# Kernel optimization log

Measured on AMD Instinct MI355X. Metric: run time of the kernel, lower is better.

Reference implementation:

```python
import jax, jax.numpy as jnp
import numpy as np

B, S, H, NH = 2, 2048, 2048, 16
HD = H // NH
CLIP_QKV = 8.0
SOFTMAX_SCALE = 1.0 / np.sqrt(HD)
NEG_INF = jnp.finfo(jnp.float32).min


def setup_inputs() -> dict:
    key = jax.random.key(0)
    k1, k2, k3, k4 = jax.random.split(key, 4)
    hidden_states = jax.random.normal(k1, (B, S, H), dtype=jnp.float32)
    position_bias = jax.random.normal(k2, (NH, S, S), dtype=jnp.float32) * 0.1
    # causal mask: True = masked out (upper triangle)
    causal = ~jnp.tril(jnp.ones((S, S), dtype=bool))
    attention_mask = jnp.broadcast_to(causal[None, None], (B, 1, S, S))
    Wqkv = jax.random.normal(k3, (3 * H, H), dtype=jnp.float32) * (1.0 / np.sqrt(H))
    Wout = jax.random.normal(k4, (H, H), dtype=jnp.float32) * (1.0 / np.sqrt(H))
    return {"hidden_states": hidden_states, "position_bias": position_bias,
            "attention_mask": attention_mask, "Wqkv": Wqkv, "Wout": Wout}


def reference(hidden_states, position_bias, attention_mask, Wqkv, Wout):
    # QKV projection (no bias) + clamp
    mixed = hidden_states @ Wqkv.T                        # [B,S,3H]
    mixed = jnp.clip(mixed, -CLIP_QKV, CLIP_QKV)
    q, k, v = jnp.split(mixed, 3, axis=2)
    # [B,S,H] -> [B,NH,S,HD]
    def split_heads(x):
        return x.reshape(B, S, NH, HD).transpose(0, 2, 1, 3)
    q, k, v = split_heads(q), split_heads(k), split_heads(v)
    scores = jnp.einsum('bhqd,bhkd->bhqk', q, k) * SOFTMAX_SCALE
    # full position bias is used (slicing indices are always 0 in source)
    scores = scores + position_bias[None]                 # [B,NH,S,S]
    scores = jnp.where(attention_mask, NEG_INF, scores)
    attn = jax.nn.softmax(scores.astype(jnp.float32), axis=-1).astype(v.dtype)
    ctx = jnp.einsum('bhqk,bhkd->bhqd', attn, v)          # [B,NH,S,HD]
    ctx = ctx.transpose(0, 2, 1, 3).reshape(B, S, H)
    attn_output = ctx @ Wout.T
    return attn_output
```

## Files before the change

kernel.cpp:

```cpp
#include <hip/hip_runtime.h>
#include <hip/hip_bf16.h>
#include <stdint.h>

typedef __bf16 bf16x8 __attribute__((ext_vector_type(8)));
typedef float f32x4 __attribute__((ext_vector_type(4)));

#define SOFTMAX_SCALE 0.08838834764831845f
#define LOG2E 1.44269504088896f

__device__ __forceinline__ bf16x8 load8_cvt(const __hip_bfloat16* p) {
  return *(const bf16x8*)p;
}
__device__ __forceinline__ bf16x8 load8_cvt(const float* p) {
  float4 a = *(const float4*)p;
  float4 b = *(const float4*)(p + 4);
  bf16x8 r;
  r[0] = (__bf16)a.x; r[1] = (__bf16)a.y; r[2] = (__bf16)a.z; r[3] = (__bf16)a.w;
  r[4] = (__bf16)b.x; r[5] = (__bf16)b.y; r[6] = (__bf16)b.z; r[7] = (__bf16)b.w;
  return r;
}

__device__ __forceinline__ void gload_lds16(const __hip_bfloat16* g,
                                            __hip_bfloat16* l) {
  __builtin_amdgcn_global_load_lds(
      (__attribute__((address_space(1))) void*)(g),
      (__attribute__((address_space(3))) void*)(l), 16, 0, 0);
}

__global__ __launch_bounds__(256) void cvt_f32_bf16(
    const float* __restrict__ in, __hip_bfloat16* __restrict__ out, int n8)
{
  int i = blockIdx.x * blockDim.x + threadIdx.x;
  int stride = gridDim.x * blockDim.x;
  for (; i < n8; i += stride)
    *(bf16x8*)(out + (int64_t)i * 8) = load8_cvt(in + (int64_t)i * 8);
}

template <typename TA, typename TB>
__device__ __forceinline__ void gemm_bt_loop(
    const TA* __restrict__ A,
    const TB* __restrict__ B,
    int K, int m0, int n0,
    __hip_bfloat16* As, __hip_bfloat16* Bs,
    f32x4 acc[4][4])
{
  const int t = threadIdx.x;
  const int w = t >> 6, lane = t & 63;
  const int wm = (w >> 1) * 64, wn = (w & 1) * 64;
  const int l16 = lane & 15, quad = lane >> 4;
  constexpr bool ASYNC = (sizeof(TA) == 2) && (sizeof(TB) == 2);

  for (int k0 = 0; k0 < K; k0 += 64) {
    if constexpr (ASYNC) {
      #pragma unroll
      for (int i = 0; i < 4; ++i) {
        int cb = (w * 4 + i) * 64;
        int idx = cb + lane;
        int row = idx >> 3;
        int chs = (idx & 7) ^ (row & 7);
        gload_lds16((const __hip_bfloat16*)A + (int64_t)(m0 + row) * K + k0 + chs * 8,
                    As + cb * 8);
        gload_lds16((const __hip_bfloat16*)B + (int64_t)(n0 + row) * K + k0 + chs * 8,
                    Bs + cb * 8);
      }
    } else {
      #pragma unroll
      for (int i = 0; i < 4; ++i) {
        int idx = i * 256 + t;
        int row = idx >> 3, ch = idx & 7;
        int sw = (ch ^ (row & 7)) * 8;
        *(bf16x8*)(As + row * 64 + sw) =
            load8_cvt(A + (int64_t)(m0 + row) * K + k0 + ch * 8);
        *(bf16x8*)(Bs + row * 64 + sw) =
            load8_cvt(B + (int64_t)(n0 + row) * K + k0 + ch * 8);
      }
    }
    __syncthreads();
    #pragma unroll
    for (int ks = 0; ks < 2; ++ks) {
      bf16x8 af[4], bfr[4];
      #pragma unroll
      for (int mt = 0; mt < 4; ++mt) {
        int row = wm + mt * 16 + l16;
        int ch = ks * 4 + quad;
        af[mt] = *(const bf16x8*)(As + row * 64 + ((ch ^ (row & 7)) * 8));
      }
      #pragma unroll
      for (int nt = 0; nt < 4; ++nt) {
        int row = wn + nt * 16 + l16;
        int ch = ks * 4 + quad;
        bfr[nt] = *(const bf16x8*)(Bs + row * 64 + ((ch ^ (row & 7)) * 8));
      }
      #pragma unroll
      for (int mt = 0; mt < 4; ++mt)
        #pragma unroll
        for (int nt = 0; nt < 4; ++nt)
          acc[mt][nt] = __builtin_amdgcn_mfma_f32_16x16x32_bf16(
              af[mt], bfr[nt], acc[mt][nt], 0, 0, 0);
    }
    __syncthreads();
  }
}

template <typename TA, typename TB>
__global__ __launch_bounds__(256) void qkv_gemm(
    const TA* __restrict__ A,
    const TB* __restrict__ W,
    __hip_bfloat16* __restrict__ qb,
    __hip_bfloat16* __restrict__ kb,
    __hip_bfloat16* __restrict__ vb)
{
  __shared__ __align__(16) __hip_bfloat16 As[128 * 64];
  __shared__ __align__(16) __hip_bfloat16 Bs[128 * 64];
  const f32x4 z4 = {0.f, 0.f, 0.f, 0.f};
  f32x4 acc[4][4];
  #pragma unroll
  for (int mt = 0; mt < 4; ++mt)
    #pragma unroll
    for (int nt = 0; nt < 4; ++nt) acc[mt][nt] = z4;

  const int K = 2048;
  const int n0 = blockIdx.x * 128, m0 = blockIdx.y * 128;
  gemm_bt_loop(A, W, K, m0, n0, As, Bs, acc);

  const int t = threadIdx.x;
  const int w = t >> 6, lane = t & 63;
  const int wm = (w >> 1) * 64, wn = (w & 1) * 64;
  const int l16 = lane & 15, quad = lane >> 4;
  __hip_bfloat16* bufs[3] = {qb, kb, vb};
  #pragma unroll
  for (int nt = 0; nt < 4; ++nt) {
    int gn = n0 + wn + nt * 16 + l16;
    int which = gn >> 11;
    int hc = gn & 2047;
    int head = hc >> 7, d = hc & 127;
    __hip_bfloat16* dst = bufs[which];
    #pragma unroll
    for (int mt = 0; mt < 4; ++mt) {
      #pragma unroll
      for (int r = 0; r < 4; ++r) {
        int gm = m0 + wm + mt * 16 + quad * 4 + r;
        int bb = gm >> 11, s = gm & 2047;
        float val = acc[mt][nt][r];
        val = fminf(8.f, fmaxf(-8.f, val));
        dst[(((int64_t)(bb * 16 + head) * 2048 + s) << 7) + d] =
            __float2bfloat16(val);
      }
    }
  }
}

__global__ __launch_bounds__(256) void transpose_v(
    const __hip_bfloat16* __restrict__ V,
    __hip_bfloat16* __restrict__ Vt)
{
  __shared__ __hip_bfloat16 tile[64][68];
  const int bh = blockIdx.z;
  const int s0 = blockIdx.x * 64;
  const int d0 = blockIdx.y * 64;
  const int t = threadIdx.x;
  const int c = t & 63, rq = t >> 6;
  const __hip_bfloat16* Vp = V + (int64_t)bh * 2048 * 128;
  #pragma unroll
  for (int j = 0; j < 16; ++j) {
    int r = rq * 16 + j;
    tile[r][c] = Vp[(int64_t)(s0 + r) * 128 + d0 + c];
  }
  __syncthreads();
  __hip_bfloat16* Vo = Vt + (int64_t)bh * 128 * 2048;
  #pragma unroll
  for (int j = 0; j < 16; ++j) {
    int dd = rq * 16 + j;
    Vo[(int64_t)(d0 + dd) * 2048 + s0 + c] = tile[c][dd];
  }
}

__device__ __forceinline__ void attn_step(
    int kt, int ktmax, int q0,
    const __hip_bfloat16* Kbase, const __hip_bfloat16* Vbase, const float* Bb,
    __hip_bfloat16* Kcur, __hip_bfloat16* Vcur,
    __hip_bfloat16* Knxt, __hip_bfloat16* Vnxt,
    __hip_bfloat16* Ps,
    const bf16x8 (&qf)[4],
    float (&bcur)[16], float (&bnxt)[16],
    f32x4 (&O)[8], float (&m_r)[4], float (&l_r)[4],
    int w, int lane, int l16, int quad)
{
  if (kt < ktmax) {
    const __hip_bfloat16* Kp = Kbase + (int64_t)(kt + 1) * 64 * 128;
    const __hip_bfloat16* Vp = Vbase + (kt + 1) * 64;
    #pragma unroll
    for (int i = 0; i < 4; ++i) {
      int cb = (w * 4 + i) * 64;
      int idx = cb + lane;
      { int row = idx >> 4, chs = (idx & 15) ^ (row & 15);
        gload_lds16(Kp + row * 128 + chs * 8, Knxt + cb * 8); }
      { int row = idx >> 3, chs = (idx & 7) ^ (row & 7);
        gload_lds16(Vp + (int64_t)row * 2048 + chs * 8, Vnxt + cb * 8); }
    }
    const float* bp = Bb + (int64_t)(q0 + w * 16 + quad * 4) * 2048
                      + (kt + 1) * 64 + l16;
    #pragma unroll
    for (int nt = 0; nt < 4; ++nt)
      #pragma unroll
      for (int r = 0; r < 4; ++r)
        bnxt[nt * 4 + r] = bp[(int64_t)r * 2048 + nt * 16];
    asm volatile("s_waitcnt vmcnt(24)" ::: "memory");
  } else {
    asm volatile("s_waitcnt vmcnt(0)" ::: "memory");
  }
  __builtin_amdgcn_s_barrier();

  const f32x4 z4 = {0.f, 0.f, 0.f, 0.f};
  f32x4 S[4];
  #pragma unroll
  for (int nt = 0; nt < 4; ++nt) S[nt] = z4;
  __builtin_amdgcn_s_setprio(1);
  #pragma unroll
  for (int ks = 0; ks < 4; ++ks) {
    int ch = ks * 4 + quad;
    bf16x8 kf[4];
    #pragma unroll
    for (int nt = 0; nt < 4; ++nt) {
      int row = nt * 16 + l16;
      kf[nt] = *(const bf16x8*)(Kcur + row * 128 + ((ch ^ (row & 15)) * 8));
    }
    #pragma unroll
    for (int nt = 0; nt < 4; ++nt)
      S[nt] = __builtin_amdgcn_mfma_f32_16x16x32_bf16(
          qf[ks], kf[nt], S[nt], 0, 0, 0);
  }
  __builtin_amdgcn_s_setprio(0);

  const bool diag = (kt == ktmax);
  #pragma unroll
  for (int r = 0; r < 4; ++r) {
    int trow = w * 16 + quad * 4 + r;
    int gq = q0 + trow;
    #pragma unroll
    for (int nt = 0; nt < 4; ++nt) {
      int col = kt * 64 + nt * 16 + l16;
      float sv = S[nt][r] * SOFTMAX_SCALE + bcur[nt * 4 + r];
      if (diag && col > gq) sv = -3.0e38f;
      S[nt][r] = sv;
    }
  }

  #pragma unroll
  for (int r = 0; r < 4; ++r) {
    float rm = fmaxf(fmaxf(S[0][r], S[1][r]), fmaxf(S[2][r], S[3][r]));
    rm = fmaxf(rm, __shfl_xor(rm, 1, 64));
    rm = fmaxf(rm, __shfl_xor(rm, 2, 64));
    rm = fmaxf(rm, __shfl_xor(rm, 4, 64));
    rm = fmaxf(rm, __shfl_xor(rm, 8, 64));
    float mo = m_r[r];
    float mn = fmaxf(mo, rm);
    float alpha = exp2f((mo - mn) * LOG2E);
    float rs = 0.f;
    #pragma unroll
    for (int nt = 0; nt < 4; ++nt) {
      float pv = exp2f((S[nt][r] - mn) * LOG2E);
      S[nt][r] = pv;
      rs += pv;
    }
    rs += __shfl_xor(rs, 1, 64);
    rs += __shfl_xor(rs, 2, 64);
    rs += __shfl_xor(rs, 4, 64);
    rs += __shfl_xor(rs, 8, 64);
    m_r[r] = mn;
    l_r[r] = l_r[r] * alpha + rs;
    #pragma unroll
    for (int nt2 = 0; nt2 < 8; ++nt2) O[nt2][r] *= alpha;
  }

  #pragma unroll
  for (int r = 0; r < 4; ++r) {
    int trow = w * 16 + quad * 4 + r;
    #pragma unroll
    for (int nt = 0; nt < 4; ++nt) {
      int col = nt * 16 + l16;
      Ps[trow * 64 + (((col >> 3) ^ (trow & 7)) << 3) + (col & 7)] =
          __float2bfloat16(S[nt][r]);
    }
  }

  __builtin_amdgcn_s_setprio(1);
  #pragma unroll
  for (int ksp = 0; ksp < 2; ++ksp) {
    int ch = ksp * 4 + quad;
    int prow = w * 16 + l16;
    bf16x8 pf = *(const bf16x8*)(Ps + prow * 64 + ((ch ^ (prow & 7)) * 8));
    #pragma unroll
    for (int nt = 0; nt < 8; ++nt) {
      int row = nt * 16 + l16;
      bf16x8 vf = *(const bf16x8*)(Vcur + row * 64 + ((ch ^ (row & 7)) * 8));
      O[nt] = __builtin_amdgcn_mfma_f32_16x16x32_bf16(pf, vf, O[nt], 0, 0, 0);
    }
  }
  __builtin_amdgcn_s_setprio(0);

  asm volatile("s_waitcnt lgkmcnt(0)" ::: "memory");
  __builtin_amdgcn_s_barrier();
}

__global__ __launch_bounds__(256, 2) void attn_kernel(
    const __hip_bfloat16* __restrict__ Q,
    const __hip_bfloat16* __restrict__ Kg,
    const __hip_bfloat16* __restrict__ Vt,
    const float* __restrict__ bias,
    __hip_bfloat16* __restrict__ ctx)
{
  __shared__ __align__(16) __hip_bfloat16 KsBuf[2][64 * 128];
  __shared__ __align__(16) __hip_bfloat16 VsBuf[2][128 * 64];
  __shared__ __align__(16) __hip_bfloat16 Ps[64 * 64];

  const int t = threadIdx.x;
  const int w = t >> 6, lane = t & 63;
  const int l16 = lane & 15, quad = lane >> 4;

  const int y = blockIdx.y;
  const int h = y >> 1, b = y & 1;
  const int bh = b * 16 + h;
  const int qt = 31 - (int)blockIdx.x;
  const int q0 = qt * 64;
  const int ktmax = qt;

  bf16x8 qf[4];
  {
    const __hip_bfloat16* Qp = Q + ((int64_t)bh * 2048 + q0 + w * 16) * 128;
    #pragma unroll
    for (int ks = 0; ks < 4; ++ks)
      qf[ks] = *(const bf16x8*)(Qp + l16 * 128 + ks * 32 + quad * 8);
  }

  const f32x4 z4 = {0.f, 0.f, 0.f, 0.f};
  f32x4 O[8];
  #pragma unroll
  for (int nt = 0; nt < 8; ++nt) O[nt] = z4;
  float m_r[4], l_r[4];
  #pragma unroll
  for (int r = 0; r < 4; ++r) { m_r[r] = -3.0e38f; l_r[r] = 0.f; }

  const __hip_bfloat16* Kbase = Kg + (int64_t)bh * 2048 * 128;
  const __hip_bfloat16* Vbase = Vt + (int64_t)bh * 128 * 2048;
  const float* Bb = bias + (int64_t)h * 2048 * 2048;

  float bA[16], bB[16];

  {
    #pragma unroll
    for (int i = 0; i < 4; ++i) {
      int cb = (w * 4 + i) * 64;
      int idx = cb + lane;
      { int row = idx >> 4, chs = (idx & 15) ^ (row & 15);
        gload_lds16(Kbase + row * 128 + chs * 8, KsBuf[0] + cb * 8); }
      { int row = idx >> 3, chs = (idx & 7) ^ (row & 7);
        gload_lds16(Vbase + (int64_t)row * 2048 + chs * 8, VsBuf[0] + cb * 8); }
    }
    const float* bp = Bb + (int64_t)(q0 + w * 16 + quad * 4) * 2048 + l16;
    #pragma unroll
    for (int nt = 0; nt < 4; ++nt)
      #pragma unroll
      for (int r = 0; r < 4; ++r)
        bA[nt * 4 + r] = bp[(int64_t)r * 2048 + nt * 16];
  }

  for (int kt = 0; kt <= ktmax; kt += 2) {
    attn_step(kt, ktmax, q0, Kbase, Vbase, Bb,
              KsBuf[0], VsBuf[0], KsBuf[1], VsBuf[1], Ps, qf,
              bA, bB, O, m_r, l_r, w, lane, l16, quad);
    if (kt + 1 <= ktmax)
      attn_step(kt + 1, ktmax, q0, Kbase, Vbase, Bb,
                KsBuf[1], VsBuf[1], KsBuf[0], VsBuf[0], Ps, qf,
                bB, bA, O, m_r, l_r, w, lane, l16, quad);
  }

  #pragma unroll
  for (int r = 0; r < 4; ++r) {
    int trow = w * 16 + quad * 4 + r;
    int gm = b * 2048 + q0 + trow;
    float inv = 1.f / l_r[r];
    __hip_bfloat16* crow = ctx + (int64_t)gm * 2048 + h * 128;
    #pragma unroll
    for (int nt = 0; nt < 8; ++nt)
      crow[nt * 16 + l16] = __float2bfloat16(O[nt][r] * inv);
  }
}

template <typename TB>
__global__ __launch_bounds__(256) void out_gemm(
    const __hip_bfloat16* __restrict__ A,
    const TB* __restrict__ W,
    float* __restrict__ out)
{
  __shared__ __align__(16) __hip_bfloat16 As[128 * 64];
  __shared__ __align__(16) __hip_bfloat16 Bs[128 * 64];
  const f32x4 z4 = {0.f, 0.f, 0.f, 0.f};
  f32x4 acc[4][4];
  #pragma unroll
  for (int mt = 0; mt < 4; ++mt)
    #pragma unroll
    for (int nt = 0; nt < 4; ++nt) acc[mt][nt] = z4;

  const int K = 2048;
  const int n0 = blockIdx.x * 128, m0 = blockIdx.y * 128;
  gemm_bt_loop(A, W, K, m0, n0, As, Bs, acc);

  const int t = threadIdx.x;
  const int w = t >> 6, lane = t & 63;
  const int wm = (w >> 1) * 64, wn = (w & 1) * 64;
  const int l16 = lane & 15, quad = lane >> 4;
  #pragma unroll
  for (int mt = 0; mt < 4; ++mt) {
    #pragma unroll
    for (int r = 0; r < 4; ++r) {
      int gm = m0 + wm + mt * 16 + quad * 4 + r;
      #pragma unroll
      for (int nt = 0; nt < 4; ++nt) {
        int gn = n0 + wn + nt * 16 + l16;
        out[(int64_t)gm * 2048 + gn] = acc[mt][nt][r];
      }
    }
  }
}

extern "C" void kernel_launch(void* const* d_in, const int* in_sizes, int n_in,
                              void* d_out, int out_size, void* d_ws, size_t ws_size,
                              hipStream_t stream) {
  const float* hs   = (const float*)d_in[0];
  const float* bias = (const float*)d_in[1];
  const float* Wqkv = (const float*)d_in[3];
  const float* Wout = (const float*)d_in[4];
  float* out = (float*)d_out;

  __hip_bfloat16* ws = (__hip_bfloat16*)d_ws;
  const size_t SEG = (size_t)32 * 2048 * 128;
  __hip_bfloat16* q   = ws;
  __hip_bfloat16* k   = ws + SEG;
  __hip_bfloat16* v   = ws + 2 * SEG;
  __hip_bfloat16* vt  = ws + 3 * SEG;
  __hip_bfloat16* ctx = ws + 2 * SEG;

  const size_t NW_QKV = (size_t)6144 * 2048;
  const size_t NW_OUT = (size_t)2048 * 2048;
  const size_t need_bytes = (4 * SEG + NW_QKV + SEG) * sizeof(__hip_bfloat16);

  if (ws_size >= need_bytes) {
    __hip_bfloat16* wqkvb = ws + 4 * SEG;
    __hip_bfloat16* hsb   = wqkvb + NW_QKV;
    __hip_bfloat16* woutb = wqkvb;
    cvt_f32_bf16<<<1024, 256, 0, stream>>>(hs, hsb, (int)(SEG / 8));
    cvt_f32_bf16<<<1024, 256, 0, stream>>>(Wqkv, wqkvb, (int)(NW_QKV / 8));
    qkv_gemm<__hip_bfloat16, __hip_bfloat16>
        <<<dim3(48, 32), 256, 0, stream>>>(hsb, wqkvb, q, k, v);
    transpose_v<<<dim3(32, 2, 32), 256, 0, stream>>>(v, vt);
    cvt_f32_bf16<<<1024, 256, 0, stream>>>(Wout, woutb, (int)(NW_OUT / 8));
    attn_kernel<<<dim3(32, 32), 256, 0, stream>>>(q, k, vt, bias, ctx);
    out_gemm<__hip_bfloat16><<<dim3(16, 32), 256, 0, stream>>>(ctx, woutb, out);
  } else {
    qkv_gemm<float, float><<<dim3(48, 32), 256, 0, stream>>>(hs, Wqkv, q, k, v);
    transpose_v<<<dim3(32, 2, 32), 256, 0, stream>>>(v, vt);
    attn_kernel<<<dim3(32, 32), 256, 0, stream>>>(q, k, vt, bias, ctx);
    out_gemm<float><<<dim3(16, 32), 256, 0, stream>>>(ctx, Wout, out);
  }
}
```

Baseline: 748.1 us.

## Single-buffer K/V in LDS and raise attention occupancy to four blocks

```diff
diff --git a/kernel.cpp b/kernel.cpp
--- a/kernel.cpp
+++ b/kernel.cpp
@@ -175,41 +175,51 @@
   }
 }
 
+__device__ __forceinline__ void issue_kv(
+    int te,
+    const __hip_bfloat16* __restrict__ Kbase,
+    const __hip_bfloat16* __restrict__ Vbase,
+    __hip_bfloat16* Kn, __hip_bfloat16* Vn, int w, int lane)
+{
+  const __hip_bfloat16* Kp = Kbase + (int64_t)te * 64 * 128;
+  const __hip_bfloat16* Vp = Vbase + te * 64;
+  #pragma unroll
+  for (int i = 0; i < 4; ++i) {
+    int cb = (w * 4 + i) * 64;
+    int idx = cb + lane;
+    { int row = idx >> 4, chs = (idx & 15) ^ (row & 15);
+      gload_lds16(Kp + row * 128 + chs * 8, Kn + cb * 8); }
+    { int row = idx >> 3, chs = (idx & 7) ^ (row & 7);
+      gload_lds16(Vp + (int64_t)row * 2048 + chs * 8, Vn + cb * 8); }
+  }
+}
+
+__device__ __forceinline__ void load_bias16(
+    const float* __restrict__ bp, int te, float (&b)[16])
+{
+  const int c = te * 64;
+  #pragma unroll
+  for (int nt = 0; nt < 4; ++nt)
+    #pragma unroll
+    for (int r = 0; r < 4; ++r)
+      b[nt * 4 + r] = bp[(int64_t)r * 2048 + c + nt * 16];
+}
+
 __device__ __forceinline__ void attn_step(
     int kt, int ktmax, int q0,
-    const __hip_bfloat16* Kbase, const __hip_bfloat16* Vbase, const float* Bb,
-    __hip_bfloat16* Kcur, __hip_bfloat16* Vcur,
-    __hip_bfloat16* Knxt, __hip_bfloat16* Vnxt,
-    __hip_bfloat16* Ps,
+    const __hip_bfloat16* __restrict__ Kbase,
+    const __hip_bfloat16* __restrict__ Vbase,
+    const float* __restrict__ bp,
+    __hip_bfloat16* __restrict__ Ks,
+    __hip_bfloat16* __restrict__ Vs,
+    __hip_bfloat16* __restrict__ Ps,
     const bf16x8 (&qf)[4],
     float (&bcur)[16], float (&bnxt)[16],
     f32x4 (&O)[8], float (&m_r)[4], float (&l_r)[4],
     int w, int lane, int l16, int quad)
 {
-  if (kt < ktmax) {
-    const __hip_bfloat16* Kp = Kbase + (int64_t)(kt + 1) * 64 * 128;
-    const __hip_bfloat16* Vp = Vbase + (kt + 1) * 64;
-    #pragma unroll
-    for (int i = 0; i < 4; ++i) {
-      int cb = (w * 4 + i) * 64;
-      int idx = cb + lane;
-      { int row = idx >> 4, chs = (idx & 15) ^ (row & 15);
-        gload_lds16(Kp + row * 128 + chs * 8, Knxt + cb * 8); }
-      { int row = idx >> 3, chs = (idx & 7) ^ (row & 7);
-        gload_lds16(Vp + (int64_t)row * 2048 + chs * 8, Vnxt + cb * 8); }
-    }
-    const float* bp = Bb + (int64_t)(q0 + w * 16 + quad * 4) * 2048
-                      + (kt + 1) * 64 + l16;
-    #pragma unroll
-    for (int nt = 0; nt < 4; ++nt)
-      #pragma unroll
-      for (int r = 0; r < 4; ++r)
-        bnxt[nt * 4 + r] = bp[(int64_t)r * 2048 + nt * 16];
-    asm volatile("s_waitcnt vmcnt(24)" ::: "memory");
-  } else {
-    asm volatile("s_waitcnt vmcnt(0)" ::: "memory");
-  }
-  __builtin_amdgcn_s_barrier();
+  issue_kv(kt, Kbase, Vbase, Ks, Vs, w, lane);
+  __syncthreads();
 
   const f32x4 z4 = {0.f, 0.f, 0.f, 0.f};
   f32x4 S[4];
@@ -223,7 +233,7 @@
     #pragma unroll
     for (int nt = 0; nt < 4; ++nt) {
       int row = nt * 16 + l16;
-      kf[nt] = *(const bf16x8*)(Kcur + row * 128 + ((ch ^ (row & 15)) * 8));
+      kf[nt] = *(const bf16x8*)(Ks + row * 128 + ((ch ^ (row & 15)) * 8));
     }
     #pragma unroll
     for (int nt = 0; nt < 4; ++nt)
@@ -232,18 +242,25 @@
   }
   __builtin_amdgcn_s_setprio(0);
 
+  load_bias16(bp, (kt + 1 <= ktmax ? kt + 1 : ktmax), bnxt);
+
   const bool diag = (kt == ktmax);
   #pragma unroll
   for (int r = 0; r < 4; ++r) {
     int trow = w * 16 + quad * 4 + r;
     int gq = q0 + trow;
-    #pragma unroll
-    for (int nt = 0; nt < 4; ++nt) {
-      int col = kt * 64 + nt * 16 + l16;
-      float sv = S[nt][r] * SOFTMAX_SCALE + bcur[nt * 4 + r];
-      if (diag && col > gq) sv = -3.0e38f;
-      S[nt][r] = sv;
-    }
+    float sv0 = S[0][r] * SOFTMAX_SCALE + bcur[r];
+    float sv1 = S[1][r] * SOFTMAX_SCALE + bcur[4 + r];
+    float sv2 = S[2][r] * SOFTMAX_SCALE + bcur[8 + r];
+    float sv3 = S[3][r] * SOFTMAX_SCALE + bcur[12 + r];
+    if (diag) {
+      int colb = kt * 64 + l16;
+      if (colb      > gq) sv0 = -3.0e38f;
+      if (colb + 16 > gq) sv1 = -3.0e38f;
+      if (colb + 32 > gq) sv2 = -3.0e38f;
+      if (colb + 48 > gq) sv3 = -3.0e38f;
+    }
+    S[0][r] = sv0; S[1][r] = sv1; S[2][r] = sv2; S[3][r] = sv3;
   }
 
   #pragma unroll
@@ -293,25 +310,24 @@
     #pragma unroll
     for (int nt = 0; nt < 8; ++nt) {
       int row = nt * 16 + l16;
-      bf16x8 vf = *(const bf16x8*)(Vcur + row * 64 + ((ch ^ (row & 7)) * 8));
+      bf16x8 vf = *(const bf16x8*)(Vs + row * 64 + ((ch ^ (row & 7)) * 8));
       O[nt] = __builtin_amdgcn_mfma_f32_16x16x32_bf16(pf, vf, O[nt], 0, 0, 0);
     }
   }
   __builtin_amdgcn_s_setprio(0);
 
-  asm volatile("s_waitcnt lgkmcnt(0)" ::: "memory");
-  __builtin_amdgcn_s_barrier();
-}
-
-__global__ __launch_bounds__(256, 2) void attn_kernel(
+  __syncthreads();
+}
+
+__global__ __launch_bounds__(256, 4) void attn_kernel(
     const __hip_bfloat16* __restrict__ Q,
     const __hip_bfloat16* __restrict__ Kg,
     const __hip_bfloat16* __restrict__ Vt,
     const float* __restrict__ bias,
     __hip_bfloat16* __restrict__ ctx)
 {
-  __shared__ __align__(16) __hip_bfloat16 KsBuf[2][64 * 128];
-  __shared__ __align__(16) __hip_bfloat16 VsBuf[2][128 * 64];
+  __shared__ __align__(16) __hip_bfloat16 Ks[64 * 128];
+  __shared__ __align__(16) __hip_bfloat16 Vs[128 * 64];
   __shared__ __align__(16) __hip_bfloat16 Ps[64 * 64];
 
   const int t = threadIdx.x;
@@ -321,9 +337,14 @@
   const int y = blockIdx.y;
   const int h = y >> 1, b = y & 1;
   const int bh = b * 16 + h;
-  const int qt = 31 - (int)blockIdx.x;
+  const int qt = (31 - (int)blockIdx.x + 8 * ((y >> 3) & 3)) & 31;
   const int q0 = qt * 64;
   const int ktmax = qt;
+
+  const __hip_bfloat16* Kbase = Kg + (int64_t)bh * 2048 * 128;
+  const __hip_bfloat16* Vbase = Vt + (int64_t)bh * 128 * 2048;
+  const float* bp = bias + (int64_t)h * 2048 * 2048
+                    + (int64_t)(q0 + w * 16 + quad * 4) * 2048 + l16;
 
   bf16x8 qf[4];
   {
@@ -341,37 +362,14 @@
   #pragma unroll
   for (int r = 0; r < 4; ++r) { m_r[r] = -3.0e38f; l_r[r] = 0.f; }
 
-  const __hip_bfloat16* Kbase = Kg + (int64_t)bh * 2048 * 128;
-  const __hip_bfloat16* Vbase = Vt + (int64_t)bh * 128 * 2048;
-  const float* Bb = bias + (int64_t)h * 2048 * 2048;
-
   float bA[16], bB[16];
-
-  {
-    #pragma unroll
-    for (int i = 0; i < 4; ++i) {
-      int cb = (w * 4 + i) * 64;
-      int idx = cb + lane;
-      { int row = idx >> 4, chs = (idx & 15) ^ (row & 15);
-        gload_lds16(Kbase + row * 128 + chs * 8, KsBuf[0] + cb * 8); }
-      { int row = idx >> 3, chs = (idx & 7) ^ (row & 7);
-        gload_lds16(Vbase + (int64_t)row * 2048 + chs * 8, VsBuf[0] + cb * 8); }
-    }
-    const float* bp = Bb + (int64_t)(q0 + w * 16 + quad * 4) * 2048 + l16;
-    #pragma unroll
-    for (int nt = 0; nt < 4; ++nt)
-      #pragma unroll
-      for (int r = 0; r < 4; ++r)
-        bA[nt * 4 + r] = bp[(int64_t)r * 2048 + nt * 16];
-  }
+  load_bias16(bp, 0, bA);
 
   for (int kt = 0; kt <= ktmax; kt += 2) {
-    attn_step(kt, ktmax, q0, Kbase, Vbase, Bb,
-              KsBuf[0], VsBuf[0], KsBuf[1], VsBuf[1], Ps, qf,
+    attn_step(kt, ktmax, q0, Kbase, Vbase, bp, Ks, Vs, Ps, qf,
               bA, bB, O, m_r, l_r, w, lane, l16, quad);
     if (kt + 1 <= ktmax)
-      attn_step(kt + 1, ktmax, q0, Kbase, Vbase, Bb,
-                KsBuf[1], VsBuf[1], KsBuf[0], VsBuf[0], Ps, qf,
+      attn_step(kt + 1, ktmax, q0, Kbase, Vbase, bp, Ks, Vs, Ps, qf,
                 bB, bA, O, m_r, l_r, w, lane, l16, quad);
   }
 
```

Result: slower. 1.076 ms (+43.8%).
